# Optimization experiments

Hardware: AMD Instinct MI355X
Metric: run time of the kernel (lower is better)

The kernel has to match this reference:

```python
import jax, jax.numpy as jnp
import numpy as np


def setup_inputs() -> dict:
    key = jax.random.key(0)
    ks = jax.random.split(key, 14)
    B, Ld, Lq, D = 64, 512, 128, 512
    d_node = jax.random.normal(ks[0], (B, Ld, D), jnp.float32)
    q_node = jax.random.normal(ks[1], (B, Lq, D), jnp.float32)
    qq_graph = jax.random.randint(ks[2], (B, Lq, Lq), 0, 2, jnp.int32)
    dq_graph = jax.random.randint(ks[3], (B, Ld, Lq), 0, 2, jnp.int32)
    dd_graph = jax.random.randint(ks[4], (B, Ld, Ld), 0, 2, jnp.int32)
    qd_graph = jax.random.randint(ks[5], (B, Lq, Ld), 0, 2, jnp.int32)
    s = 0.02
    W_nw = jax.random.normal(ks[6], (1, D), jnp.float32) * s
    b_nw = jnp.zeros((1,), jnp.float32)
    W_self = jax.random.normal(ks[7], (D, D), jnp.float32) * s
    b_self = jnp.zeros((D,), jnp.float32)
    W_dd = jax.random.normal(ks[8], (D, D), jnp.float32) * s
    W_qq = jax.random.normal(ks[9], (D, D), jnp.float32) * s
    W_dq = jax.random.normal(ks[10], (D, D), jnp.float32) * s
    W_qd = jax.random.normal(ks[11], (D, D), jnp.float32) * s
    return {"d_node": d_node, "q_node": q_node, "qq_graph": qq_graph,
            "dq_graph": dq_graph, "dd_graph": dd_graph, "qd_graph": qd_graph,
            "W_nw": W_nw, "b_nw": b_nw, "W_self": W_self, "b_self": b_self,
            "W_dd": W_dd, "W_qq": W_qq, "W_dq": W_dq, "W_qd": W_qd,
            "iteration_steps": 2}


def reference(d_node, q_node, qq_graph, dq_graph, dd_graph, qd_graph,
              W_nw, b_nw, W_self, b_self, W_dd, W_qq, W_dq, W_qd,
              iteration_steps):
    dd = dd_graph.astype(jnp.float32)
    dq = dq_graph.astype(jnp.float32)
    qq = qq_graph.astype(jnp.float32)
    qd = qd_graph.astype(jnp.float32)

    # neighbor counts, clamped to 1 where a node has no neighbors
    d_nb = dd.sum(-1) + dq.sum(-1)              # [B, Ld]
    d_nb = jnp.where(d_nb >= 1.0, d_nb, 1.0)
    q_nb = qq.sum(-1) + qd.sum(-1)              # [B, Lq]
    q_nb = jnp.where(q_nb >= 1.0, q_nb, 1.0)

    all_d_w, all_q_w = [], []
    for _ in range(iteration_steps):
        d_w = jax.nn.sigmoid(jnp.einsum('bld,od->blo', d_node, W_nw) + b_nw)[..., 0]  # [B, Ld]
        q_w = jax.nn.sigmoid(jnp.einsum('bld,od->blo', q_node, W_nw) + b_nw)[..., 0]  # [B, Lq]
        all_d_w.append(d_w)
        all_q_w.append(q_w)

        self_d = jnp.einsum('bld,od->blo', d_node, W_self) + b_self
        self_q = jnp.einsum('bld,od->blo', q_node, W_self) + b_self
        dd_info = jnp.einsum('bld,od->blo', d_node, W_dd)
        qd_info = jnp.einsum('bld,od->blo', d_node, W_qd)
        qq_info = jnp.einsum('bld,od->blo', q_node, W_qq)
        dq_info = jnp.einsum('bld,od->blo', q_node, W_dq)

        # masked weights: graph is 0/1, so replace_masked_values(., graph, 0) == graph * weight
        dd_msg = jnp.einsum('bij,bjd->bid', dd * d_w[:, None, :], dd_info)  # [B,Ld,D]
        qd_msg = jnp.einsum('bij,bjd->bid', qd * d_w[:, None, :], qd_info)  # [B,Lq,D]
        qq_msg = jnp.einsum('bij,bjd->bid', qq * q_w[:, None, :], qq_info)  # [B,Lq,D]
        dq_msg = jnp.einsum('bij,bjd->bid', dq * q_w[:, None, :], dq_info)  # [B,Ld,D]

        agg_q = (qq_msg + qd_msg) / q_nb[..., None]
        agg_d = (dd_msg + dq_msg) / d_nb[..., None]
        d_node = jax.nn.relu(self_d + agg_d)
        q_node = jax.nn.relu(self_q + agg_q)

    all_d_w = jnp.stack(all_d_w, axis=1)  # [B, steps, Ld]
    all_q_w = jnp.stack(all_q_w, axis=1)  # [B, steps, Lq]
    return (d_node, q_node, all_d_w, all_q_w)
```

## Files before the change

kernel.cpp:

```cpp
#include <hip/hip_runtime.h>
#include <cstdint>
#include <cstddef>

typedef _Float16 h16;
typedef __attribute__((ext_vector_type(8))) _Float16 h16x8;
typedef __attribute__((ext_vector_type(4))) _Float16 h16x4;
typedef __attribute__((ext_vector_type(4))) float f32x4;

constexpr int B_ = 64, LD = 512, LQ = 128, DIM = 512, STEPS = 2;
constexpr int MD = B_ * LD;
constexpr int MQ = B_ * LQ;
constexpr int KST = LD + LQ;
constexpr int KAGG = KST + DIM;

#define ASYNC16(gp, lp)                                                          \
  __builtin_amdgcn_global_load_lds(                                              \
      (const __attribute__((address_space(1))) unsigned int*)(gp),               \
      (__attribute__((address_space(3))) unsigned int*)(lp), 16, 0, 0)

struct Src {
  const h16* p0; int s0; long bstr0;
  const h16* p1; int s1; long bstr1;
  int ksplit;
};

template <int WM, int WN, class Epi>
__device__ __forceinline__ void gemm_body(int b, long tileM, long tileN,
                                          Src sa, Src sb, int K,
                                          const Epi& epi, h16* lds) {
  constexpr int BM = WM * 32;
  constexpr int BN = WN * 64;
  constexpr int AE = BM * 32;
  constexpr int BUFE = (BM + BN) * 32;
  constexpr int NA = BM / 128;
  constexpr int NB = BN / 128;
  constexpr int HM = WM / 2;

  const int tid = threadIdx.x;
  const int lane = tid & 63;
  const int wv = tid >> 6;
  const int wr = wv >> 2, wc = wv & 3;
  const int quad = lane >> 4, l16 = lane & 15;

  const int u = tid & 255;
  const int sb2 = tid >> 8;
  const int r = u >> 2;
  const int es = (r ^ (r >> 2)) & 3;
  const int kq = (u & 3) ^ es;

  const h16* pa[2][NA];
  const h16* pb[2][NB];
#pragma unroll
  for (int s = 0; s < NA; s++) {
    const long row = tileM + sb2 * 64 + r + 128 * s;
    pa[0][s] = sa.p0 + (size_t)b * sa.bstr0 + row * (long)sa.s0 + kq * 8;
    pa[1][s] = sa.p1 + (size_t)b * sa.bstr1 + row * (long)sa.s1 + kq * 8 - sa.ksplit;
  }
#pragma unroll
  for (int s = 0; s < NB; s++) {
    const long row = tileN + sb2 * 64 + r + 128 * s;
    pb[0][s] = sb.p0 + (size_t)b * sb.bstr0 + row * (long)sb.s0 + kq * 8;
    pb[1][s] = sb.p1 + (size_t)b * sb.bstr1 + row * (long)sb.s1 + kq * 8 - sb.ksplit;
  }

  const int ef = (l16 ^ (l16 >> 2)) & 3;
  int offA[WM], offB[WN];
#pragma unroll
  for (int i = 0; i < WM; i++) {
    const int row = wr * (WM * 16) + i * 16 + l16;
    offA[i] = (row * 4 + (quad ^ ef)) * 8;
  }
#pragma unroll
  for (int j = 0; j < WN; j++) {
    const int row = wc * (WN * 16) + j * 16 + l16;
    offB[j] = AE + (row * 4 + (quad ^ ef)) * 8;
  }

  f32x4 acc[WM][WN] = {};
  const int T = K >> 5;

  auto dmaA = [&](int t, int off) {
    const int k0 = t * 32;
    h16* base = lds + off + tid * 8;
    const int sel = (k0 >= sa.ksplit);
#pragma unroll
    for (int s = 0; s < NA; s++) ASYNC16(pa[sel][s] + k0, base + 4096 * s);
  };
  auto dmaB = [&](int t, int off) {
    const int k0 = t * 32;
    h16* base = lds + off + AE + tid * 8;
    const int sel = (k0 >= sb.ksplit);
#pragma unroll
    for (int s = 0; s < NB; s++) ASYNC16(pb[sel][s] + k0, base + 4096 * s);
  };

  h16x8 af0[HM], af1[WM - HM], bf[WN];

  dmaA(0, 0); dmaB(0, 0);
  dmaA(1, BUFE); dmaB(1, BUFE);
  if constexpr (NA == 2) asm volatile("s_waitcnt vmcnt(4)" ::: "memory");
  else                   asm volatile("s_waitcnt vmcnt(2)" ::: "memory");
  __builtin_amdgcn_s_barrier();

  int co = 0;
  int no = 2 * BUFE;
  for (int t = 0; t < T; ++t) {
    const bool pf = (t + 2 < T);
#pragma unroll
    for (int j = 0; j < WN; j++) bf[j] = *(const h16x8*)(lds + co + offB[j]);
#pragma unroll
    for (int i = 0; i < HM; i++) af0[i] = *(const h16x8*)(lds + co + offA[i]);
    if (pf) dmaA(t + 2, no);
    __builtin_amdgcn_sched_barrier(0);
    __builtin_amdgcn_s_barrier();
    asm volatile("s_waitcnt lgkmcnt(0)" ::: "memory");
    __builtin_amdgcn_sched_barrier(0);
    __builtin_amdgcn_s_setprio(1);
#pragma unroll
    for (int i = 0; i < HM; i++)
#pragma unroll
      for (int j = 0; j < WN; j++)
        acc[i][j] = __builtin_amdgcn_mfma_f32_16x16x32_f16(af0[i], bf[j], acc[i][j], 0, 0, 0);
    __builtin_amdgcn_s_setprio(0);
    __builtin_amdgcn_sched_barrier(0);
    __builtin_amdgcn_s_barrier();
    if (pf) {
      if constexpr (NA == 2) asm volatile("s_waitcnt vmcnt(2)" ::: "memory");
      else                   asm volatile("s_waitcnt vmcnt(1)" ::: "memory");
    } else {
      asm volatile("s_waitcnt vmcnt(0)" ::: "memory");
    }
#pragma unroll
    for (int i = 0; i < WM - HM; i++) af1[i] = *(const h16x8*)(lds + co + offA[HM + i]);
    if (pf) dmaB(t + 2, no);
    __builtin_amdgcn_sched_barrier(0);
    __builtin_amdgcn_s_barrier();
    asm volatile("s_waitcnt lgkmcnt(0)" ::: "memory");
    __builtin_amdgcn_sched_barrier(0);
    __builtin_amdgcn_s_setprio(1);
#pragma unroll
    for (int i = 0; i < WM - HM; i++)
#pragma unroll
      for (int j = 0; j < WN; j++)
        acc[HM + i][j] = __builtin_amdgcn_mfma_f32_16x16x32_f16(af1[i], bf[j], acc[HM + i][j], 0, 0, 0);
    __builtin_amdgcn_s_setprio(0);
    __builtin_amdgcn_sched_barrier(0);
    __builtin_amdgcn_s_barrier();

    co = (co == 2 * BUFE) ? 0 : co + BUFE;
    no = (no == 2 * BUFE) ? 0 : no + BUFE;
  }

#pragma unroll
  for (int i = 0; i < WM; i++) {
#pragma unroll
    for (int j = 0; j < WN; j++) {
      const int gm0 = (int)tileM + wr * (WM * 16) + i * 16 + quad * 4;
      const int gn  = (int)tileN + wc * (WN * 16) + j * 16 + l16;
#pragma unroll
      for (int rr = 0; rr < 4; rr++) epi(b, gm0 + rr, gn, acc[i][j][rr]);
    }
  }
}

struct EpiDense {
  const float* w;
  h16* stackA;
  h16* stackB;
  int lnShift;
  int offA, offB;
  __device__ void operator()(int, int gm, int gn, float v) const {
    const int b = gn >> lnShift, l = gn & ((1 << lnShift) - 1);
    const h16 sv = (h16)(w[gn] * v);
    if (gm < 512)
      stackA[((size_t)b * 512 + gm) * 640 + offA + l] = sv;
    else
      stackB[((size_t)b * 512 + (gm - 512)) * 640 + offB + l] = sv;
  }
};
struct EpiAgg {
  const float* bias;
  float* out;
  h16* nodeNext;
  int rowsPerB;
  __device__ void operator()(int b, int gm, int gn, float v) const {
    const size_t row = (size_t)b * rowsPerB + gm;
    const float val = fmaxf(v + bias[gn], 0.f);
    if (out) out[row * 512 + gn] = val;
    if (nodeNext) nodeNext[row * 512 + gn] = (h16)val;
  }
};

__global__ __launch_bounds__(512, 2) void k_dense(Src saD, Src sbD, EpiDense epiD,
                                                  Src saQ, Src sbQ, EpiDense epiQ) {
  __shared__ __align__(16) h16 lds[3 * (256 * 32 + 256 * 32)];
  const int g = blockIdx.x;
  const int x = g / 160;
  const int yy = g % 160;
  if (yy < 128)
    gemm_body<8, 4>(0, (long)x * 256, (long)yy * 256, saD, sbD, 512, epiD, lds);
  else
    gemm_body<8, 4>(0, (long)x * 256, (long)(yy - 128) * 256, saQ, sbQ, 512, epiQ, lds);
}

__global__ __launch_bounds__(512, 2) void k_agg(Src saD, Src sbD, EpiAgg epiD,
                                                Src saQ, Src sbQ, EpiAgg epiQ) {
  __shared__ __align__(16) h16 lds[3 * (256 * 32 + 256 * 32)];
  const int g = blockIdx.x;
  const int b = g & 63;
  const int unit = g >> 6;
  if (unit < 4)
    gemm_body<8, 4>(b, (long)(unit >> 1) * 256, (long)(unit & 1) * 256, saD, sbD, KAGG, epiD, lds);
  else
    gemm_body<4, 2>(b, 0L, (long)(unit - 4) * 128, saQ, sbQ, KAGG, epiQ, lds);
}

__global__ __launch_bounds__(256) void k_convert(const float* __restrict__ dn,
                                                 const float* __restrict__ qn,
                                                 h16* __restrict__ dnb,
                                                 h16* __restrict__ qnb) {
  const size_t i4 = ((size_t)blockIdx.x * 256 + threadIdx.x) * 4;
  constexpr size_t TD = (size_t)MD * DIM;
  const float* src; h16* dst; size_t idx;
  if (i4 < TD) { src = dn; dst = dnb; idx = i4; }
  else         { src = qn; dst = qnb; idx = i4 - TD; }
  const float4 v = *(const float4*)&src[idx];
  h16x4 o; o.x = (h16)v.x; o.y = (h16)v.y; o.z = (h16)v.z; o.w = (h16)v.w;
  *(h16x4*)&dst[idx] = o;
}

__global__ __launch_bounds__(256) void k_wcat(const float* __restrict__ Wself,
                                              const float* __restrict__ Wdd,
                                              const float* __restrict__ Wqd,
                                              const float* __restrict__ Wqq,
                                              const float* __restrict__ Wdq,
                                              h16* __restrict__ catD,
                                              h16* __restrict__ catQ) {
  const int i = blockIdx.x * 256 + threadIdx.x;
  float vD, vQ;
  if (i < 512 * 512)       { vD = Wself[i];            vQ = vD; }
  else if (i < 1024 * 512) { vD = Wdd[i - 512 * 512];  vQ = Wqq[i - 512 * 512]; }
  else                     { vD = Wqd[i - 1024 * 512]; vQ = Wdq[i - 1024 * 512]; }
  catD[i] = (h16)vD; catQ[i] = (h16)vQ;
}

__global__ __launch_bounds__(256) void k_maskD(const int* __restrict__ dd,
                                               const int* __restrict__ dq,
                                               h16* __restrict__ maskD) {
  const int row = blockIdx.x * 4 + (threadIdx.x >> 6);
  const int lane = threadIdx.x & 63;
  const int* pdd = dd + (size_t)row * 512;
  const int* pdq = dq + (size_t)row * 128;
  h16* pm = maskD + (size_t)row * 640;
  float vals[10];
  float s = 0.f;
#pragma unroll
  for (int t = 0; t < 10; t++) {
    const int j = lane + t * 64;
    const float v = (float)((j < 512) ? pdd[j] : pdq[j - 512]);
    vals[t] = v; s += v;
  }
  for (int m = 32; m; m >>= 1) s += __shfl_xor(s, m);
  const float inv = 1.f / fmaxf(s, 1.f);
#pragma unroll
  for (int t = 0; t < 10; t++) pm[lane + t * 64] = (h16)(vals[t] * inv);
}

__global__ __launch_bounds__(256) void k_maskQ(const int* __restrict__ qq,
                                               const int* __restrict__ qd,
                                               h16* __restrict__ maskQ) {
  const int row = blockIdx.x * 4 + (threadIdx.x >> 6);
  const int lane = threadIdx.x & 63;
  const int* pqq = qq + (size_t)row * 128;
  const int* pqd = qd + (size_t)row * 512;
  h16* pm = maskQ + (size_t)row * 640;
  float vals[10];
  float s = 0.f;
#pragma unroll
  for (int t = 0; t < 10; t++) {
    const int j = lane + t * 64;
    const float v = (float)((j < 128) ? pqq[j] : pqd[j - 128]);
    vals[t] = v; s += v;
  }
  for (int m = 32; m; m >>= 1) s += __shfl_xor(s, m);
  const float inv = 1.f / fmaxf(s, 1.f);
#pragma unroll
  for (int t = 0; t < 10; t++) pm[lane + t * 64] = (h16)(vals[t] * inv);
}

__global__ __launch_bounds__(256) void k_w(const h16* __restrict__ dnb,
                                           const h16* __restrict__ qnb,
                                           const float* __restrict__ Wnw,
                                           const float* __restrict__ bnw,
                                           float* __restrict__ d_w,
                                           float* __restrict__ q_w,
                                           float* __restrict__ adw,
                                           float* __restrict__ aqw, int it) {
  const int row = blockIdx.x * 4 + (threadIdx.x >> 6);
  const int lane = threadIdx.x & 63;
  const bool isD = row < MD;
  const h16* node = isD ? dnb + (size_t)row * 512 : qnb + (size_t)(row - MD) * 512;
  const h16x8 v = *(const h16x8*)&node[lane * 8];
  const float4 w0 = *(const float4*)&Wnw[lane * 8];
  const float4 w1 = *(const float4*)&Wnw[lane * 8 + 4];
  float s = (float)v[0] * w0.x + (float)v[1] * w0.y + (float)v[2] * w0.z +
            (float)v[3] * w0.w + (float)v[4] * w1.x + (float)v[5] * w1.y +
            (float)v[6] * w1.z + (float)v[7] * w1.w;
  for (int m = 32; m; m >>= 1) s += __shfl_xor(s, m);
  if (lane == 0) {
    const float w = 1.f / (1.f + expf(-(s + bnw[0])));
    if (isD) {
      d_w[row] = w;
      adw[((size_t)(row >> 9) * STEPS + it) * 512 + (row & 511)] = w;
    } else {
      const int rq = row - MD;
      q_w[rq] = w;
      aqw[((size_t)(rq >> 7) * STEPS + it) * 128 + (rq & 127)] = w;
    }
  }
}

extern "C" void kernel_launch(void* const* d_in, const int* in_sizes, int n_in,
                              void* d_out, int out_size, void* d_ws, size_t ws_size,
                              hipStream_t stream) {
  (void)in_sizes; (void)n_in; (void)out_size; (void)ws_size;

  const float* d_node = (const float*)d_in[0];
  const float* q_node = (const float*)d_in[1];
  const int*   qq     = (const int*)d_in[2];
  const int*   dq     = (const int*)d_in[3];
  const int*   dd     = (const int*)d_in[4];
  const int*   qd     = (const int*)d_in[5];
  const float* W_nw   = (const float*)d_in[6];
  const float* b_nw   = (const float*)d_in[7];
  const float* W_self = (const float*)d_in[8];
  const float* b_self = (const float*)d_in[9];
  const float* W_dd   = (const float*)d_in[10];
  const float* W_qq   = (const float*)d_in[11];
  const float* W_dq   = (const float*)d_in[12];
  const float* W_qd   = (const float*)d_in[13];

  float* outd = (float*)d_out;
  float* outq = outd + (size_t)MD * DIM;
  float* adw  = outq + (size_t)MQ * DIM;
  float* aqw  = adw + (size_t)B_ * STEPS * LD;

  char* p = (char*)d_ws;
  auto alloc = [&](size_t bytes) { char* r = p; p += (bytes + 255) & ~(size_t)255; return r; };
  h16* dnode[2], *qnode[2];
  dnode[0] = (h16*)alloc((size_t)MD * DIM * 2);
  dnode[1] = (h16*)alloc((size_t)MD * DIM * 2);
  qnode[0] = (h16*)alloc((size_t)MQ * DIM * 2);
  qnode[1] = (h16*)alloc((size_t)MQ * DIM * 2);
  h16* catD    = (h16*)alloc((size_t)1536 * 512 * 2);
  h16* catQ    = (h16*)alloc((size_t)1536 * 512 * 2);
  h16* maskD   = (h16*)alloc((size_t)B_ * LD * KST * 2);
  h16* maskQ   = (h16*)alloc((size_t)B_ * LQ * KST * 2);
  h16* stackDT = (h16*)alloc((size_t)B_ * 512 * KST * 2);
  h16* stackQT = (h16*)alloc((size_t)B_ * 512 * KST * 2);
  float* d_wb  = (float*)alloc((size_t)MD * 4);
  float* q_wb  = (float*)alloc((size_t)MQ * 4);

  k_convert<<<dim3((MD * DIM + MQ * DIM) / 4 / 256), 256, 0, stream>>>(d_node, q_node, dnode[0], qnode[0]);
  k_wcat<<<dim3(1536 * 512 / 256), 256, 0, stream>>>(W_self, W_dd, W_qd, W_qq, W_dq, catD, catQ);
  k_maskD<<<dim3(MD / 4), 256, 0, stream>>>(dd, dq, maskD);
  k_maskQ<<<dim3(MQ / 4), 256, 0, stream>>>(qq, qd, maskQ);

  for (int it = 0; it < STEPS; it++) {
    const bool last = (it == STEPS - 1);
    h16* ncur_d = dnode[it & 1];
    h16* nnext_d = dnode[(it & 1) ^ 1];
    h16* ncur_q = qnode[it & 1];
    h16* nnext_q = qnode[(it & 1) ^ 1];

    k_w<<<dim3((MD + MQ) / 4), 256, 0, stream>>>(ncur_d, ncur_q, W_nw, b_nw, d_wb, q_wb, adw, aqw, it);

    {
      Src saD{catD + 512 * 512, 512, 0, catD + 512 * 512, 512, 0, 512};
      Src sbD{ncur_d, 512, 0, ncur_d, 512, 0, 512};
      Src saQ{catQ + 512 * 512, 512, 0, catQ + 512 * 512, 512, 0, 512};
      Src sbQ{ncur_q, 512, 0, ncur_q, 512, 0, 512};
      k_dense<<<dim3(640), 512, 0, stream>>>(
          saD, sbD, EpiDense{d_wb, stackDT, stackQT, 9, 0, 128},
          saQ, sbQ, EpiDense{q_wb, stackQT, stackDT, 7, 0, 512});
    }
    {
      Src saD{maskD, 640, (long)LD * KST, ncur_d, 512, (long)LD * DIM, KST};
      Src sbD{stackDT, 640, (long)512 * KST, catD, 512, 0, KST};
      Src saQ{maskQ, 640, (long)LQ * KST, ncur_q, 512, (long)LQ * DIM, KST};
      Src sbQ{stackQT, 640, (long)512 * KST, catQ, 512, 0, KST};
      k_agg<<<dim3(512), 512, 0, stream>>>(
          saD, sbD, EpiAgg{b_self, last ? outd : nullptr, last ? nullptr : nnext_d, 512},
          saQ, sbQ, EpiAgg{b_self, last ? outq : nullptr, last ? nullptr : nnext_q, 128});
    }
  }
}
```

Baseline: 576.4 us.

## Switch GEMM mainloop to double-buffered 64-wide K stages

Replaces the triple-buffered 32-wide K pipeline, which split A and B loads into separate half-phases, with a double buffer holding 64-wide K stages made of two 32-wide slices. Each iteration issues the async loads for the next stage, then runs two MFMA phases over the current stage, halving the number of loop iterations and barrier rounds per unit of K. The cost is waiting for all outstanding loads (vmcnt(0)) at the end of every iteration, so prefetch depth drops to one stage. LDS per block grows from 96KB to 128KB, which may affect the two-blocks-per-CU occupancy target.

Result: no change. 575.6 us (-0.1%).

```diff
diff --git a/kernel.cpp b/kernel.cpp
--- a/kernel.cpp
+++ b/kernel.cpp
@@ -30,11 +30,11 @@
                                           const Epi& epi, h16* lds) {
   constexpr int BM = WM * 32;
   constexpr int BN = WN * 64;
-  constexpr int AE = BM * 32;
-  constexpr int BUFE = (BM + BN) * 32;
+  constexpr int ASL = BM * 32;
+  constexpr int BSL = BN * 32;
+  constexpr int BUFE = 2 * (ASL + BSL);
   constexpr int NA = BM / 128;
   constexpr int NB = BN / 128;
-  constexpr int HM = WM / 2;
 
   const int tid = threadIdx.x;
   const int lane = tid & 63;
@@ -73,82 +73,63 @@
 #pragma unroll
   for (int j = 0; j < WN; j++) {
     const int row = wc * (WN * 16) + j * 16 + l16;
-    offB[j] = AE + (row * 4 + (quad ^ ef)) * 8;
+    offB[j] = (row * 4 + (quad ^ ef)) * 8;
   }
 
   f32x4 acc[WM][WN] = {};
-  const int T = K >> 5;
-
-  auto dmaA = [&](int t, int off) {
-    const int k0 = t * 32;
-    h16* base = lds + off + tid * 8;
-    const int sel = (k0 >= sa.ksplit);
-#pragma unroll
-    for (int s = 0; s < NA; s++) ASYNC16(pa[sel][s] + k0, base + 4096 * s);
+  const int T = K >> 6;
+
+  auto dmaStage = [&](int t, int off) {
+#pragma unroll
+    for (int sl = 0; sl < 2; sl++) {
+      const int k0 = t * 64 + sl * 32;
+      {
+        h16* base = lds + off + sl * ASL + tid * 8;
+        const int se = (k0 >= sa.ksplit);
+#pragma unroll
+        for (int s = 0; s < NA; s++) ASYNC16(pa[se][s] + k0, base + 4096 * s);
+      }
+      {
+        h16* base = lds + off + 2 * ASL + sl * BSL + tid * 8;
+        const int se = (k0 >= sb.ksplit);
+#pragma unroll
+        for (int s = 0; s < NB; s++) ASYNC16(pb[se][s] + k0, base + 4096 * s);
+      }
+    }
   };
-  auto dmaB = [&](int t, int off) {
-    const int k0 = t * 32;
-    h16* base = lds + off + AE + tid * 8;
-    const int sel = (k0 >= sb.ksplit);
-#pragma unroll
-    for (int s = 0; s < NB; s++) ASYNC16(pb[sel][s] + k0, base + 4096 * s);
+  auto phase = [&](int off, int sl) {
+    h16x8 af[WM], bf[WN];
+    const int ab = off + sl * ASL;
+    const int bb = off + 2 * ASL + sl * BSL;
+#pragma unroll
+    for (int j = 0; j < WN; j++) bf[j] = *(const h16x8*)(lds + bb + offB[j]);
+#pragma unroll
+    for (int i = 0; i < WM; i++) af[i] = *(const h16x8*)(lds + ab + offA[i]);
+    __builtin_amdgcn_s_setprio(1);
+#pragma unroll
+    for (int i = 0; i < WM; i++)
+#pragma unroll
+      for (int j = 0; j < WN; j++)
+        acc[i][j] = __builtin_amdgcn_mfma_f32_16x16x32_f16(af[i], bf[j], acc[i][j], 0, 0, 0);
+    __builtin_amdgcn_s_setprio(0);
   };
 
-  h16x8 af0[HM], af1[WM - HM], bf[WN];
-
-  dmaA(0, 0); dmaB(0, 0);
-  dmaA(1, BUFE); dmaB(1, BUFE);
-  if constexpr (NA == 2) asm volatile("s_waitcnt vmcnt(4)" ::: "memory");
-  else                   asm volatile("s_waitcnt vmcnt(2)" ::: "memory");
-  __builtin_amdgcn_s_barrier();
+  dmaStage(0, 0);
+  asm volatile("s_waitcnt vmcnt(0)" ::: "memory");
 
   int co = 0;
-  int no = 2 * BUFE;
   for (int t = 0; t < T; ++t) {
-    const bool pf = (t + 2 < T);
-#pragma unroll
-    for (int j = 0; j < WN; j++) bf[j] = *(const h16x8*)(lds + co + offB[j]);
-#pragma unroll
-    for (int i = 0; i < HM; i++) af0[i] = *(const h16x8*)(lds + co + offA[i]);
-    if (pf) dmaA(t + 2, no);
+    __builtin_amdgcn_s_barrier();
+    asm volatile("" ::: "memory");
     __builtin_amdgcn_sched_barrier(0);
+    if (t + 1 < T) dmaStage(t + 1, co ^ BUFE);
+    phase(co, 0);
     __builtin_amdgcn_s_barrier();
-    asm volatile("s_waitcnt lgkmcnt(0)" ::: "memory");
+    asm volatile("" ::: "memory");
     __builtin_amdgcn_sched_barrier(0);
-    __builtin_amdgcn_s_setprio(1);
-#pragma unroll
-    for (int i = 0; i < HM; i++)
-#pragma unroll
-      for (int j = 0; j < WN; j++)
-        acc[i][j] = __builtin_amdgcn_mfma_f32_16x16x32_f16(af0[i], bf[j], acc[i][j], 0, 0, 0);
-    __builtin_amdgcn_s_setprio(0);
-    __builtin_amdgcn_sched_barrier(0);
-    __builtin_amdgcn_s_barrier();
-    if (pf) {
-      if constexpr (NA == 2) asm volatile("s_waitcnt vmcnt(2)" ::: "memory");
-      else                   asm volatile("s_waitcnt vmcnt(1)" ::: "memory");
-    } else {
-      asm volatile("s_waitcnt vmcnt(0)" ::: "memory");
-    }
-#pragma unroll
-    for (int i = 0; i < WM - HM; i++) af1[i] = *(const h16x8*)(lds + co + offA[HM + i]);
-    if (pf) dmaB(t + 2, no);
-    __builtin_amdgcn_sched_barrier(0);
-    __builtin_amdgcn_s_barrier();
-    asm volatile("s_waitcnt lgkmcnt(0)" ::: "memory");
-    __builtin_amdgcn_sched_barrier(0);
-    __builtin_amdgcn_s_setprio(1);
-#pragma unroll
-    for (int i = 0; i < WM - HM; i++)
-#pragma unroll
-      for (int j = 0; j < WN; j++)
-        acc[HM + i][j] = __builtin_amdgcn_mfma_f32_16x16x32_f16(af1[i], bf[j], acc[HM + i][j], 0, 0, 0);
-    __builtin_amdgcn_s_setprio(0);
-    __builtin_amdgcn_sched_barrier(0);
-    __builtin_amdgcn_s_barrier();
-
-    co = (co == 2 * BUFE) ? 0 : co + BUFE;
-    no = (no == 2 * BUFE) ? 0 : no + BUFE;
+    phase(co, 1);
+    asm volatile("s_waitcnt vmcnt(0)" ::: "memory");
+    co ^= BUFE;
   }
 
 #pragma unroll
@@ -193,7 +174,7 @@
 
 __global__ __launch_bounds__(512, 2) void k_dense(Src saD, Src sbD, EpiDense epiD,
                                                   Src saQ, Src sbQ, EpiDense epiQ) {
-  __shared__ __align__(16) h16 lds[3 * (256 * 32 + 256 * 32)];
+  __shared__ __align__(16) h16 lds[2 * ((256 + 256) * 64)];
   const int g = blockIdx.x;
   const int x = g / 160;
   const int yy = g % 160;
@@ -205,7 +186,7 @@
 
 __global__ __launch_bounds__(512, 2) void k_agg(Src saD, Src sbD, EpiAgg epiD,
                                                 Src saQ, Src sbQ, EpiAgg epiQ) {
-  __shared__ __align__(16) h16 lds[3 * (256 * 32 + 256 * 32)];
+  __shared__ __align__(16) h16 lds[2 * ((256 + 256) * 64)];
   const int g = blockIdx.x;
   const int b = g & 63;
   const int unit = g >> 6;
```
